# Performance work log

Hardware: AMD Instinct MI355X
Metric: run time of the kernel (lower is better)

The kernel has to match this reference:

```python
import jax, jax.numpy as jnp
import numpy as np

D = 768        # d_model
NH = 12        # n_head
HD = D // NH   # head_dim = 64
T = 8          # num_frames
SCALE = 1.0
LN_EPS = 1e-5


def _layer_norm(x, g, b):
    # fp16-safe LayerNorm: compute in fp32, cast back (matches LayerNorm subclass)
    x32 = x.astype(jnp.float32)
    mu = jnp.mean(x32, axis=-1, keepdims=True)
    var = jnp.mean(jnp.square(x32 - mu), axis=-1, keepdims=True)
    y = (x32 - mu) / jnp.sqrt(var + LN_EPS) * g + b
    return y.astype(x.dtype)


def _adapter(x, w1, b1, w2, b2):
    # Adapter with skip_connect=False: fc1 -> exact GELU -> fc2
    h = jax.nn.gelu(x @ w1.T + b1, approximate=False)
    return h @ w2.T + b2


def _mha(xq, ykv, w_in, b_in, w_out, b_out, need_weights=False):
    # xq: (Tx, N, D), ykv: (Ty, N, D); manual in-proj split like the torch code
    q = xq @ w_in[:D].T + b_in[:D]
    k = ykv @ w_in[D:2 * D].T + b_in[D:2 * D]
    v = ykv @ w_in[2 * D:].T + b_in[2 * D:]
    Tx, N = q.shape[0], q.shape[1]
    Ty = k.shape[0]
    q = q.reshape(Tx, N, NH, HD).transpose(1, 2, 0, 3)  # (N, H, Tx, hd)
    k = k.reshape(Ty, N, NH, HD).transpose(1, 2, 0, 3)
    v = v.reshape(Ty, N, NH, HD).transpose(1, 2, 0, 3)
    aff = jnp.einsum('nhqd,nhkd->nhqk', q, k) / jnp.asarray(HD ** 0.5, q.dtype)
    if need_weights:
        # torch does this under no_grad: sum over heads, exp, sum over (Tx*Ty)
        w = jax.lax.stop_gradient(
            jnp.sum(jnp.exp(jnp.sum(aff, axis=1)).reshape(N, -1), axis=-1))
    p = jax.nn.softmax(aff, axis=-1)
    out = jnp.einsum('nhqk,nhkd->nhqd', p, v)
    out = out.transpose(2, 0, 1, 3).reshape(Tx, N, D)
    out = out @ w_out.T + b_out
    if need_weights:
        return out, w
    return out


def setup_inputs() -> dict:
    key = jax.random.key(0)
    ks = jax.random.split(key, 12)
    DH = D // 4  # adapter hidden = 192

    def w(k, shape):
        return jax.random.normal(k, shape, jnp.float32) * 0.02

    z = lambda *s: jnp.zeros(s, jnp.float32)
    return {
        'x': jax.random.normal(ks[0], (197, 64, D), jnp.float32),
        'in_proj_w': w(ks[1], (3 * D, D)), 'in_proj_b': z(3 * D),
        'out_proj_w': w(ks[2], (D, D)), 'out_proj_b': z(D),
        'ln1_g': jnp.ones((D,), jnp.float32), 'ln1_b': z(D),
        'ln2_g': jnp.ones((D,), jnp.float32), 'ln2_b': z(D),
        'fc_w': w(ks[3], (4 * D, D)), 'fc_b': z(4 * D),
        'proj_w': w(ks[4], (D, 4 * D)), 'proj_b': z(D),
        'sa1_w': w(ks[5], (DH, D)), 'sa1_b': z(DH),
        'sa2_w': w(ks[6], (D, DH)), 'sa2_b': z(D),
        'ta1_w': w(ks[7], (DH, D)), 'ta1_b': z(DH),
        'ta2_w': w(ks[8], (D, DH)), 'ta2_b': z(D),
        'ma1_w': w(ks[9], (DH, D)), 'ma1_b': z(DH),
        'ma2_w': w(ks[10], (D, DH)), 'ma2_b': z(D),
    }


def reference(x, in_proj_w, in_proj_b, out_proj_w, out_proj_b,
              ln1_g, ln1_b, ln2_g, ln2_b, fc_w, fc_b, proj_w, proj_b,
              sa1_w, sa1_b, sa2_w, sa2_b, ta1_w, ta1_b, ta2_w, ta2_b,
              ma1_w, ma1_b, ma2_w, ma2_b):
    n, bt, d = x.shape
    b = bt // T
    # temporal attention on the class token: 'n (b t) d -> t (b n) d'
    ct = x[0]                                   # (bt, d)
    xt = ct.reshape(b, T, d).transpose(1, 0, 2)  # (T, b, d)
    xt = _mha(_layer_norm(xt, ln1_g, ln1_b), _layer_norm(xt, ln1_g, ln1_b),
              in_proj_w, in_proj_b, out_proj_w, out_proj_b)
    xt = _adapter(xt, ta1_w, ta1_b, ta2_w, ta2_b)
    xt = xt.transpose(1, 0, 2).reshape(1, bt, d)  # 't (b n) d -> n (b t) d'

    xln = _layer_norm(x, ln1_g, ln1_b)
    ori_attn, ori_w = _mha(xln, xln, in_proj_w, in_proj_b,
                           out_proj_w, out_proj_b, need_weights=True)
    crs_attn, crs_w = _mha(xln, xt, in_proj_w, in_proj_b,
                           out_proj_w, out_proj_b, need_weights=True)
    lam = (crs_w / (crs_w + ori_w))[None, :, None]  # (1, bt, 1)
    x = x + (1.0 - lam) * ori_attn \
          + SCALE * _adapter(lam * crs_attn, sa1_w, sa1_b, sa2_w, sa2_b)

    xn = _layer_norm(x, ln2_g, ln2_b)
    h = xn @ fc_w.T + fc_b
    h = h * jax.nn.sigmoid(1.702 * h)  # QuickGELU
    mlp_out = h @ proj_w.T + proj_b
    x = x + mlp_out + SCALE * _adapter(xn, ma1_w, ma1_b, ma2_w, ma2_b)
    return x
```

## Files before the change

### kernel.cpp

```cpp
#include <hip/hip_runtime.h>
#include <hip/hip_bf16.h>
#include <math.h>


typedef __attribute__((ext_vector_type(8))) short bf16x8;
typedef __attribute__((ext_vector_type(4))) float f32x4;

__device__ __forceinline__ float bf2f(short s) {
  unsigned u = ((unsigned)(unsigned short)s) << 16;
  float f;
  __builtin_memcpy(&f, &u, 4);
  return f;
}
__device__ __forceinline__ short f2bf(float f) {
  __hip_bfloat16 h = __float2bfloat16(f);
  short s;
  __builtin_memcpy(&s, &h, 2);
  return s;
}

__device__ __forceinline__ void gld16(void* lds, const void* g) {
  __builtin_amdgcn_global_load_lds(
      (const __attribute__((address_space(1))) unsigned int*)g,
      (__attribute__((address_space(3))) unsigned int*)lds, 16, 0, 0);
}

struct WPair { const float* s; short* d; int n; };
struct WArr { WPair p[10]; };

__global__ __launch_bounds__(256)
void convert_k(WArr a) {
  WPair w = a.p[blockIdx.y];
  for (int i = blockIdx.x * 256 + threadIdx.x; i < w.n; i += gridDim.x * 256)
    w.d[i] = f2bf(w.s[i]);
}

__global__ __launch_bounds__(256)
void ln_k(const float* __restrict__ in, const float* __restrict__ g,
          const float* __restrict__ b, short* __restrict__ out) {
  const int t = blockIdx.x;
  const float* xr = in + (size_t)t * 768;
  const int tid = threadIdx.x;
  float v0 = xr[tid], v1 = xr[tid + 256], v2 = xr[tid + 512];
  float s = v0 + v1 + v2;
#pragma unroll
  for (int m = 1; m < 64; m <<= 1) s += __shfl_xor(s, m);
  __shared__ float red[4];
  if ((tid & 63) == 0) red[tid >> 6] = s;
  __syncthreads();
  float mu = (red[0] + red[1] + red[2] + red[3]) * (1.f / 768.f);
  __syncthreads();
  float d0 = v0 - mu, d1 = v1 - mu, d2 = v2 - mu;
  float q = d0 * d0 + d1 * d1 + d2 * d2;
#pragma unroll
  for (int m = 1; m < 64; m <<= 1) q += __shfl_xor(q, m);
  if ((tid & 63) == 0) red[tid >> 6] = q;
  __syncthreads();
  float rstd = rsqrtf((red[0] + red[1] + red[2] + red[3]) * (1.f / 768.f) + 1e-5f);
  size_t o = (size_t)t * 768;
  out[o + tid]       = f2bf(d0 * rstd * g[tid]       + b[tid]);
  out[o + tid + 256] = f2bf(d1 * rstd * g[tid + 256] + b[tid + 256]);
  out[o + tid + 512] = f2bf(d2 * rstd * g[tid + 512] + b[tid + 512]);
}

template <int ACT, int EPI>
__global__ __launch_bounds__(256)
void gemm_k(const short* __restrict__ A, int lda,
            const short* __restrict__ W,
            const float* __restrict__ bias,
            short* __restrict__ outb, float* __restrict__ outf,
            const float* __restrict__ lam,
            int M, int N, int K) {
  __shared__ short As[64][40];
  __shared__ short Ws[64][40];
  const int tid = threadIdx.x;
  const int n0 = blockIdx.x * 64;
  const int m0 = blockIdx.y * 64;
  const int lane = tid & 63, w = tid >> 6;
  const int wr = w >> 1, wc = w & 1;
  const int g = lane >> 4, li = lane & 15;
  const int srow = tid >> 2, scol = (tid & 3) * 8;

  f32x4 acc[2][2];
#pragma unroll
  for (int i = 0; i < 2; i++)
#pragma unroll
    for (int j = 0; j < 2; j++) acc[i][j] = (f32x4){0.f, 0.f, 0.f, 0.f};

  const short* Aptr = A + (size_t)(m0 + srow) * lda + scol;
  const short* Wptr = W + (size_t)(n0 + srow) * K + scol;

  for (int kk = 0; kk < K; kk += 32) {
    __syncthreads();
    *(bf16x8*)&As[srow][scol] = *(const bf16x8*)(Aptr + kk);
    *(bf16x8*)&Ws[srow][scol] = *(const bf16x8*)(Wptr + kk);
    __syncthreads();
    bf16x8 a[2], b[2];
#pragma unroll
    for (int mi = 0; mi < 2; ++mi)
      a[mi] = *(const bf16x8*)&As[wr * 32 + mi * 16 + li][g * 8];
#pragma unroll
    for (int ni = 0; ni < 2; ++ni)
      b[ni] = *(const bf16x8*)&Ws[wc * 32 + ni * 16 + li][g * 8];
#pragma unroll
    for (int mi = 0; mi < 2; ++mi)
#pragma unroll
      for (int ni = 0; ni < 2; ++ni)
        acc[mi][ni] = __builtin_amdgcn_mfma_f32_16x16x32_bf16(
            a[mi], b[ni], acc[mi][ni], 0, 0, 0);
  }

#pragma unroll
  for (int mi = 0; mi < 2; ++mi)
#pragma unroll
    for (int ni = 0; ni < 2; ++ni)
#pragma unroll
      for (int r = 0; r < 4; ++r) {
        int row = m0 + wr * 32 + mi * 16 + g * 4 + r;
        int col = n0 + wc * 32 + ni * 16 + li;
        float v = acc[mi][ni][r];
        if (bias) v += bias[col];
        if (ACT == 1) v = v / (1.f + __expf(-1.702f * v));
        if (ACT == 2) v = 0.5f * v * (1.f + erff(v * 0.70710678118f));
        size_t idx = (size_t)row * N + col;
        if (EPI == 0) outb[idx] = f2bf(v);
        else if (EPI == 1) outf[idx] = v;
        else if (EPI == 5) outb[idx] = f2bf(v * lam[row]);
      }
}

template <int ACT, int EPI>
__global__ __launch_bounds__(256)
void gemm128_k(const short* __restrict__ A, int lda,
               const short* __restrict__ W,
               const float* __restrict__ bias,
               short* __restrict__ outb, float* __restrict__ outf,
               const float* __restrict__ lam,
               const float* __restrict__ addv,
               const float* __restrict__ resid,
               const short* __restrict__ A2, int lda2,
               const short* __restrict__ W2,
               const float* __restrict__ bias2, int K2,
               int M, int N, int K, int nx) {
  int nwg = gridDim.x;
  int orig = blockIdx.x;
  int q = nwg >> 3, r = nwg & 7;
  int xcd = orig & 7, cidx = orig >> 3;
  int wgid = (xcd < r ? xcd * (q + 1) : r * (q + 1) + (xcd - r) * q) + cidx;
  const int n0 = (wgid % nx) * 128;
  const int m0 = (wgid / nx) * 128;

  __shared__ short As[128][32];
  __shared__ short Ws[128][32];
  const int tid = threadIdx.x;
  const int w = tid >> 6, lane = tid & 63;
  const int g = lane >> 4, li = lane & 15;
  const int wr = w >> 1, wc = w & 1;

  const int srow = w * 16 + (lane >> 2);
  const int scol = (lane & 3) * 8;

  f32x4 acc[4][4];
#pragma unroll
  for (int i = 0; i < 4; i++)
#pragma unroll
    for (int j = 0; j < 4; j++) acc[i][j] = (f32x4){0.f, 0.f, 0.f, 0.f};

  int ar0 = m0 + srow;       if (ar0 > M - 1) ar0 = M - 1;
  int ar1 = m0 + 64 + srow;  if (ar1 > M - 1) ar1 = M - 1;
  const short* Ap0 = A + (size_t)ar0 * lda + scol;
  const short* Ap1 = A + (size_t)ar1 * lda + scol;
  const short* Wp0 = W + (size_t)(n0 + srow) * K + scol;
  const short* Wp1 = W + (size_t)(n0 + 64 + srow) * K + scol;
  short* lA0 = &As[w * 16][0];
  short* lA1 = &As[64 + w * 16][0];
  short* lW0 = &Ws[w * 16][0];
  short* lW1 = &Ws[64 + w * 16][0];

  for (int kk = 0; kk < K; kk += 32) {
    __syncthreads();
    gld16(lA0, Ap0 + kk);
    gld16(lA1, Ap1 + kk);
    gld16(lW0, Wp0 + kk);
    gld16(lW1, Wp1 + kk);
    __syncthreads();
    bf16x8 a[4], b[4];
#pragma unroll
    for (int mi = 0; mi < 4; ++mi)
      a[mi] = *(const bf16x8*)&As[wr * 64 + mi * 16 + li][g * 8];
#pragma unroll
    for (int ni = 0; ni < 4; ++ni)
      b[ni] = *(const bf16x8*)&Ws[wc * 64 + ni * 16 + li][g * 8];
#pragma unroll
    for (int mi = 0; mi < 4; ++mi)
#pragma unroll
      for (int ni = 0; ni < 4; ++ni)
        acc[mi][ni] = __builtin_amdgcn_mfma_f32_16x16x32_bf16(
            a[mi], b[ni], acc[mi][ni], 0, 0, 0);
  }

  if (A2) {
    const short* Bp0 = A2 + (size_t)ar0 * lda2 + scol;
    const short* Bp1 = A2 + (size_t)ar1 * lda2 + scol;
    const short* Vp0 = W2 + (size_t)(n0 + srow) * K2 + scol;
    const short* Vp1 = W2 + (size_t)(n0 + 64 + srow) * K2 + scol;
    for (int kk = 0; kk < K2; kk += 32) {
      __syncthreads();
      gld16(lA0, Bp0 + kk);
      gld16(lA1, Bp1 + kk);
      gld16(lW0, Vp0 + kk);
      gld16(lW1, Vp1 + kk);
      __syncthreads();
      bf16x8 a[4], b[4];
#pragma unroll
      for (int mi = 0; mi < 4; ++mi)
        a[mi] = *(const bf16x8*)&As[wr * 64 + mi * 16 + li][g * 8];
#pragma unroll
      for (int ni = 0; ni < 4; ++ni)
        b[ni] = *(const bf16x8*)&Ws[wc * 64 + ni * 16 + li][g * 8];
#pragma unroll
      for (int mi = 0; mi < 4; ++mi)
#pragma unroll
        for (int ni = 0; ni < 4; ++ni)
          acc[mi][ni] = __builtin_amdgcn_mfma_f32_16x16x32_bf16(
              a[mi], b[ni], acc[mi][ni], 0, 0, 0);
    }
  }

#pragma unroll
  for (int mi = 0; mi < 4; ++mi)
#pragma unroll
    for (int ni = 0; ni < 4; ++ni)
#pragma unroll
      for (int r = 0; r < 4; ++r) {
        int row = m0 + wr * 64 + mi * 16 + g * 4 + r;
        int col = n0 + wc * 64 + ni * 16 + li;
        if (row >= M) continue;
        float v = acc[mi][ni][r];
        if (bias) v += bias[col];
        if (bias2) v += bias2[col];
        if (ACT == 1) v = v / (1.f + __expf(-1.702f * v));
        if (ACT == 2) v = 0.5f * v * (1.f + erff(v * 0.70710678118f));
        size_t idx = (size_t)row * N + col;
        if (EPI == 0) outb[idx] = f2bf(v);
        else if (EPI == 2) {
          float l = lam[row & 63];
          outf[idx] = resid[idx] + (1.f - l) * v + addv[(size_t)(row & 63) * 768 + col];
        } else if (EPI == 6) outf[idx] = resid[idx] + v;
      }
}

__global__ __launch_bounds__(256)
void attn_k(const short* __restrict__ qkv, short* __restrict__ attn_out) {
  const int n = blockIdx.x;
  const int h = blockIdx.y;
  const int tid = threadIdx.x;
  const int lane = tid & 63, w = tid >> 6;
  const int g = lane >> 4, li = lane & 15;

  __shared__ short Vt[64][232];
  __shared__ short Pl[4][16][232];

  {
    const int d = tid & 63;
    for (int key = tid >> 6; key < 224; key += 4) {
      short v = 0;
      if (key < 197)
        v = qkv[(size_t)(key * 64 + n) * 2304 + 1536 + h * 64 + d];
      Vt[d][key] = v;
    }
  }
  __syncthreads();

  const short* Qb = qkv + (size_t)n * 2304 + h * 64;
  const short* Kb = Qb + 768;

  for (int mt = w; mt < 13; mt += 4) {
    const int m0 = mt * 16;
    int arow = m0 + li;
    if (arow > 196) arow = 196;
    bf16x8 a0 = *(const bf16x8*)(Qb + (size_t)arow * 147456 + g * 8);
    bf16x8 a1 = *(const bf16x8*)(Qb + (size_t)arow * 147456 + 32 + g * 8);

    float s[13][4];
#pragma unroll
    for (int nt = 0; nt < 13; ++nt) {
      int kc = nt * 16 + li;
      if (kc > 196) kc = 196;
      bf16x8 b0 = *(const bf16x8*)(Kb + (size_t)kc * 147456 + g * 8);
      bf16x8 b1 = *(const bf16x8*)(Kb + (size_t)kc * 147456 + 32 + g * 8);
      f32x4 acc = (f32x4){0.f, 0.f, 0.f, 0.f};
      acc = __builtin_amdgcn_mfma_f32_16x16x32_bf16(a0, b0, acc, 0, 0, 0);
      acc = __builtin_amdgcn_mfma_f32_16x16x32_bf16(a1, b1, acc, 0, 0, 0);
#pragma unroll
      for (int r = 0; r < 4; ++r) s[nt][r] = acc[r] * 0.125f;
    }

#pragma unroll
    for (int r = 0; r < 4; ++r) {
      float mx = -1e30f;
#pragma unroll
      for (int nt = 0; nt < 13; ++nt) {
        if (nt * 16 + li >= 197) s[nt][r] = -1e30f;
        mx = fmaxf(mx, s[nt][r]);
      }
      mx = fmaxf(mx, __shfl_xor(mx, 1));
      mx = fmaxf(mx, __shfl_xor(mx, 2));
      mx = fmaxf(mx, __shfl_xor(mx, 4));
      mx = fmaxf(mx, __shfl_xor(mx, 8));
      float sum = 0.f;
#pragma unroll
      for (int nt = 0; nt < 13; ++nt) {
        float e = (s[nt][r] <= -1e29f) ? 0.f : __expf(s[nt][r] - mx);
        s[nt][r] = e;
        sum += e;
      }
      sum += __shfl_xor(sum, 1);
      sum += __shfl_xor(sum, 2);
      sum += __shfl_xor(sum, 4);
      sum += __shfl_xor(sum, 8);
      float inv = 1.f / sum;
#pragma unroll
      for (int nt = 0; nt < 13; ++nt) s[nt][r] *= inv;
    }

#pragma unroll
    for (int r = 0; r < 4; ++r) {
      int row = g * 4 + r;
#pragma unroll
      for (int nt = 0; nt < 13; ++nt)
        Pl[w][row][nt * 16 + li] = f2bf(s[nt][r]);
      Pl[w][row][208 + li] = 0;
    }
    asm volatile("s_waitcnt lgkmcnt(0)" ::: "memory");
    __builtin_amdgcn_sched_barrier(0);

    f32x4 o[4];
#pragma unroll
    for (int ni = 0; ni < 4; ++ni) o[ni] = (f32x4){0.f, 0.f, 0.f, 0.f};
#pragma unroll
    for (int kk = 0; kk < 7; ++kk) {
      bf16x8 pa = *(const bf16x8*)&Pl[w][li][kk * 32 + g * 8];
#pragma unroll
      for (int ni = 0; ni < 4; ++ni) {
        bf16x8 vb = *(const bf16x8*)&Vt[ni * 16 + li][kk * 32 + g * 8];
        o[ni] = __builtin_amdgcn_mfma_f32_16x16x32_bf16(pa, vb, o[ni], 0, 0, 0);
      }
    }
#pragma unroll
    for (int ni = 0; ni < 4; ++ni)
#pragma unroll
      for (int r = 0; r < 4; ++r) {
        int prow = m0 + g * 4 + r;
        if (prow < 197)
          attn_out[(size_t)(prow * 64 + n) * 768 + h * 64 + ni * 16 + li] =
              f2bf(o[ni][r]);
      }
  }
}

__global__ __launch_bounds__(256)
void lam_part_k(const short* __restrict__ qkv, float* __restrict__ eo_part) {
  const int n = blockIdx.x;
  const int mt = blockIdx.y;
  const int tid = threadIdx.x;
  const int lane = tid & 63, w = tid >> 6;
  const int g = lane >> 4, li = lane & 15;
  const short* Qb = qkv + (size_t)n * 2304;
  const short* Kb = Qb + 768;

  int arow = mt * 16 + li;
  if (arow > 196) arow = 196;
  const short* Ap = Qb + (size_t)arow * 147456;

  bf16x8 a[24];
#pragma unroll
  for (int s = 0; s < 24; ++s)
    a[s] = *(const bf16x8*)(Ap + s * 32 + g * 8);

  float eo = 0.f;
  for (int nt = w; nt < 13; nt += 4) {
    int kc = nt * 16 + li;
    if (kc > 196) kc = 196;
    const short* Bp = Kb + (size_t)kc * 147456;
    f32x4 acc = (f32x4){0.f, 0.f, 0.f, 0.f};
#pragma unroll
    for (int s = 0; s < 24; ++s) {
      bf16x8 b = *(const bf16x8*)(Bp + s * 32 + g * 8);
      acc = __builtin_amdgcn_mfma_f32_16x16x32_bf16(a[s], b, acc, 0, 0, 0);
    }
#pragma unroll
    for (int r = 0; r < 4; ++r) {
      int prow = mt * 16 + g * 4 + r;
      int col = nt * 16 + li;
      if (prow < 197 && col < 197) eo += __expf(acc[r] * 0.125f);
    }
  }

#pragma unroll
  for (int m = 1; m < 64; m <<= 1) eo += __shfl_xor(eo, m);
  __shared__ float red[4];
  if (lane == 0) red[w] = eo;
  __syncthreads();
  if (tid == 0)
    eo_part[n * 13 + mt] = red[0] + red[1] + red[2] + red[3];
}

__global__ __launch_bounds__(64)
void lam_fin_k(const short* __restrict__ qkv, const short* __restrict__ kvt,
               const float* __restrict__ eo_part, float* __restrict__ lam) {
  const int n = blockIdx.x;
  const int lane = threadIdx.x;
  const short* kt = kvt + (size_t)n * 1536;

  float ec = 0.f;
  for (int p = lane; p < 197; p += 64) {
    const short* qp = qkv + (size_t)n * 2304 + (size_t)p * 147456;
    float dot = 0.f;
    for (int d0 = 0; d0 < 768; d0 += 8) {
      bf16x8 qa = *(const bf16x8*)(qp + d0);
      bf16x8 ka = *(const bf16x8*)(kt + d0);
#pragma unroll
      for (int j = 0; j < 8; ++j) dot += bf2f(qa[j]) * bf2f(ka[j]);
    }
    ec += __expf(dot * 0.125f);
  }
#pragma unroll
  for (int m = 1; m < 64; m <<= 1) ec += __shfl_xor(ec, m);

  if (lane == 0) {
    float eo = 0.f;
#pragma unroll
    for (int t = 0; t < 13; ++t) eo += eo_part[n * 13 + t];
    lam[n] = ec / (ec + eo);
  }
}

__global__ __launch_bounds__(64)
void tattn_k(const short* __restrict__ qkv, short* __restrict__ attn_t) {
  const int bb = blockIdx.x, h = blockIdx.y;
  const int tid = threadIdx.x;
  __shared__ float sm[8][9];
  {
    const int tt = tid >> 3, ss = tid & 7;
    const short* q = qkv + (size_t)(bb * 8 + tt) * 2304 + h * 64;
    const short* k = qkv + (size_t)(bb * 8 + ss) * 2304 + 768 + h * 64;
    float dot = 0.f;
#pragma unroll
    for (int d = 0; d < 64; d += 8) {
      bf16x8 qa = *(const bf16x8*)(q + d);
      bf16x8 ka = *(const bf16x8*)(k + d);
#pragma unroll
      for (int j = 0; j < 8; ++j) dot += bf2f(qa[j]) * bf2f(ka[j]);
    }
    sm[tt][ss] = dot * 0.125f;
  }
  __syncthreads();
  if (tid < 8) {
    float mx = -1e30f;
#pragma unroll
    for (int s2 = 0; s2 < 8; ++s2) mx = fmaxf(mx, sm[tid][s2]);
    float sum = 0.f;
#pragma unroll
    for (int s2 = 0; s2 < 8; ++s2) {
      float e = __expf(sm[tid][s2] - mx);
      sm[tid][s2] = e;
      sum += e;
    }
    float inv = 1.f / sum;
#pragma unroll
    for (int s2 = 0; s2 < 8; ++s2) sm[tid][s2] *= inv;
  }
  __syncthreads();
  {
    const int d = tid;
    float v[8];
#pragma unroll
    for (int s2 = 0; s2 < 8; ++s2)
      v[s2] = bf2f(qkv[(size_t)(bb * 8 + s2) * 2304 + 1536 + h * 64 + d]);
#pragma unroll
    for (int tt = 0; tt < 8; ++tt) {
      float o = 0.f;
#pragma unroll
      for (int s2 = 0; s2 < 8; ++s2) o += sm[tt][s2] * v[s2];
      attn_t[(size_t)(bb * 8 + tt) * 768 + h * 64 + d] = f2bf(o);
    }
  }
}

extern "C" void kernel_launch(void* const* d_in, const int* in_sizes, int n_in,
                              void* d_out, int out_size, void* d_ws,
                              size_t ws_size, hipStream_t stream) {
  (void)in_sizes; (void)n_in; (void)out_size; (void)ws_size;

  const float* x          = (const float*)d_in[0];
  const float* in_proj_w  = (const float*)d_in[1];
  const float* in_proj_b  = (const float*)d_in[2];
  const float* out_proj_w = (const float*)d_in[3];
  const float* out_proj_b = (const float*)d_in[4];
  const float* ln1_g      = (const float*)d_in[5];
  const float* ln1_b      = (const float*)d_in[6];
  const float* ln2_g      = (const float*)d_in[7];
  const float* ln2_b      = (const float*)d_in[8];
  const float* fc_w       = (const float*)d_in[9];
  const float* fc_b       = (const float*)d_in[10];
  const float* proj_w     = (const float*)d_in[11];
  const float* proj_b     = (const float*)d_in[12];
  const float* sa1_w      = (const float*)d_in[13];
  const float* sa1_b      = (const float*)d_in[14];
  const float* sa2_w      = (const float*)d_in[15];
  const float* sa2_b      = (const float*)d_in[16];
  const float* ta1_w      = (const float*)d_in[17];
  const float* ta1_b      = (const float*)d_in[18];
  const float* ta2_w      = (const float*)d_in[19];
  const float* ta2_b      = (const float*)d_in[20];
  const float* ma1_w      = (const float*)d_in[21];
  const float* ma1_b      = (const float*)d_in[22];
  const float* ma2_w      = (const float*)d_in[23];
  const float* ma2_b      = (const float*)d_in[24];

  char* ws = (char*)d_ws;
  short* xln  = (short*)(ws + 0);
  short* qkv  = (short*)(ws + 19365888);
  short* hbuf = (short*)(ws + 0);
  short* attn = (short*)(ws + 77463552);
  short* h2   = (short*)(ws + 77463552);
  float* x1   = (float*)(ws + 96829440);
  short* xn   = (short*)(ws + 135561216);

  char* wreg = ws + 154927104;
  short* w_inproj  = (short*)(wreg + 0);
  short* w_outproj = (short*)(wreg + 3538944);
  short* w_fc      = (short*)(wreg + 4718592);
  short* w_proj    = (short*)(wreg + 9437184);
  short* w_sa1     = (short*)(wreg + 14155776);
  short* w_sa2     = (short*)(wreg + 14450688);
  short* w_ta1     = (short*)(wreg + 14745600);
  short* w_ta2     = (short*)(wreg + 15040512);
  short* w_ma1     = (short*)(wreg + 15335424);
  short* w_ma2     = (short*)(wreg + 15630336);

  char* sm = ws + 170852352;
  short* attn_t  = (short*)(sm + 0);
  short* tproj   = (short*)(sm + 98304);
  short* th      = (short*)(sm + 196608);
  short* xt_out  = (short*)(sm + 221184);
  short* kv_t    = (short*)(sm + 319488);
  short* a_in    = (short*)(sm + 516096);
  short* sa_h    = (short*)(sm + 614400);
  float* sa_out  = (float*)(sm + 638976);
  float* lam     = (float*)(sm + 835584);
  float* eo_part = (float*)(sm + 835840);

  float* out = (float*)d_out;

  WArr arr;
  arr.p[0] = {in_proj_w,  w_inproj,  2304 * 768};
  arr.p[1] = {out_proj_w, w_outproj, 768 * 768};
  arr.p[2] = {fc_w,       w_fc,      3072 * 768};
  arr.p[3] = {proj_w,     w_proj,    768 * 3072};
  arr.p[4] = {sa1_w,      w_sa1,     192 * 768};
  arr.p[5] = {sa2_w,      w_sa2,     768 * 192};
  arr.p[6] = {ta1_w,      w_ta1,     192 * 768};
  arr.p[7] = {ta2_w,      w_ta2,     768 * 192};
  arr.p[8] = {ma1_w,      w_ma1,     192 * 768};
  arr.p[9] = {ma2_w,      w_ma2,     768 * 192};
  convert_k<<<dim3(128, 10), 256, 0, stream>>>(arr);

  ln_k<<<12608, 256, 0, stream>>>(x, ln1_g, ln1_b, xln);

  gemm128_k<0, 0><<<18 * 99, 256, 0, stream>>>(
      xln, 768, w_inproj, in_proj_b, qkv, nullptr, nullptr, nullptr, nullptr,
      nullptr, 0, nullptr, nullptr, 0, 12608, 2304, 768, 18);

  lam_part_k<<<dim3(64, 13), 256, 0, stream>>>(qkv, eo_part);

  tattn_k<<<dim3(8, 12), 64, 0, stream>>>(qkv, attn_t);

  gemm_k<0, 0><<<dim3(12, 1), 256, 0, stream>>>(
      attn_t, 768, w_outproj, out_proj_b, tproj, nullptr, nullptr, 64, 768, 768);
  gemm_k<2, 0><<<dim3(3, 1), 256, 0, stream>>>(
      tproj, 768, w_ta1, ta1_b, th, nullptr, nullptr, 64, 192, 768);
  gemm_k<0, 0><<<dim3(12, 1), 256, 0, stream>>>(
      th, 192, w_ta2, ta2_b, xt_out, nullptr, nullptr, 64, 768, 192);
  gemm_k<0, 0><<<dim3(24, 1), 256, 0, stream>>>(
      xt_out, 768, w_inproj + 768 * 768, in_proj_b + 768, kv_t, nullptr,
      nullptr, 64, 1536, 768);

  attn_k<<<dim3(64, 12), 256, 0, stream>>>(qkv, attn);

  lam_fin_k<<<64, 64, 0, stream>>>(qkv, kv_t, eo_part, lam);

  gemm_k<0, 5><<<dim3(12, 1), 256, 0, stream>>>(
      kv_t + 768, 1536, w_outproj, out_proj_b, a_in, nullptr, lam, 64, 768, 768);
  gemm_k<2, 0><<<dim3(3, 1), 256, 0, stream>>>(
      a_in, 768, w_sa1, sa1_b, sa_h, nullptr, nullptr, 64, 192, 768);
  gemm_k<0, 1><<<dim3(12, 1), 256, 0, stream>>>(
      sa_h, 192, w_sa2, sa2_b, nullptr, sa_out, nullptr, 64, 768, 192);

  gemm128_k<0, 2><<<6 * 99, 256, 0, stream>>>(
      attn, 768, w_outproj, out_proj_b, nullptr, x1, lam, sa_out, x,
      nullptr, 0, nullptr, nullptr, 0, 12608, 768, 768, 6);

  ln_k<<<12608, 256, 0, stream>>>(x1, ln2_g, ln2_b, xn);

  gemm128_k<1, 0><<<24 * 99, 256, 0, stream>>>(
      xn, 768, w_fc, fc_b, hbuf, nullptr, nullptr, nullptr, nullptr,
      nullptr, 0, nullptr, nullptr, 0, 12608, 3072, 768, 24);
  gemm_k<2, 0><<<dim3(3, 197), 256, 0, stream>>>(
      xn, 768, w_ma1, ma1_b, h2, nullptr, nullptr, 12608, 192, 768);

  gemm128_k<0, 6><<<6 * 99, 256, 0, stream>>>(
      hbuf, 3072, w_proj, proj_b, nullptr, out, nullptr, nullptr, x1,
      h2, 192, w_ma2, ma2_b, 192, 12608, 768, 3072, 6);
}
```

Measured before the change: 761.6 us.

## Triple-buffer LDS in the 128x128 GEMM with async prefetch two stages ahead

The 128-tile GEMM now uses three LDS buffers and issues global-to-LDS loads two k-steps ahead. Per-step waits use vmcnt counting and a single barrier instead of two __syncthreads. The second (adapter) K-loop is merged into the same pipelined loop through a unified stage index. The goal is to hide global load latency behind MFMA work, at the cost of triple the LDS footprint, which may reduce occupancy.

```diff
diff --git a/kernel.cpp b/kernel.cpp
--- a/kernel.cpp
+++ b/kernel.cpp
@@ -131,17 +131,17 @@
 
 template <int ACT, int EPI>
 __global__ __launch_bounds__(256)
-void gemm128_k(const short* __restrict__ A, int lda,
-               const short* __restrict__ W,
-               const float* __restrict__ bias,
-               short* __restrict__ outb, float* __restrict__ outf,
-               const float* __restrict__ lam,
-               const float* __restrict__ addv,
-               const float* __restrict__ resid,
-               const short* __restrict__ A2, int lda2,
-               const short* __restrict__ W2,
-               const float* __restrict__ bias2, int K2,
-               int M, int N, int K, int nx) {
+void gemm128p_k(const short* __restrict__ A, int lda,
+                const short* __restrict__ W,
+                const float* __restrict__ bias,
+                short* __restrict__ outb, float* __restrict__ outf,
+                const float* __restrict__ lam,
+                const float* __restrict__ addv,
+                const float* __restrict__ resid,
+                const short* __restrict__ A2, int lda2,
+                const short* __restrict__ W2,
+                const float* __restrict__ bias2, int K2,
+                int M, int N, int K, int nx) {
   int nwg = gridDim.x;
   int orig = blockIdx.x;
   int q = nwg >> 3, r = nwg & 7;
@@ -150,8 +150,8 @@
   const int n0 = (wgid % nx) * 128;
   const int m0 = (wgid / nx) * 128;
 
-  __shared__ short As[128][32];
-  __shared__ short Ws[128][32];
+  __shared__ short As[3][128][32];
+  __shared__ short Ws[3][128][32];
   const int tid = threadIdx.x;
   const int w = tid >> 6, lane = tid & 63;
   const int g = lane >> 4, li = lane & 15;
@@ -172,59 +172,64 @@
   const short* Ap1 = A + (size_t)ar1 * lda + scol;
   const short* Wp0 = W + (size_t)(n0 + srow) * K + scol;
   const short* Wp1 = W + (size_t)(n0 + 64 + srow) * K + scol;
-  short* lA0 = &As[w * 16][0];
-  short* lA1 = &As[64 + w * 16][0];
-  short* lW0 = &Ws[w * 16][0];
-  short* lW1 = &Ws[64 + w * 16][0];
-
-  for (int kk = 0; kk < K; kk += 32) {
-    __syncthreads();
-    gld16(lA0, Ap0 + kk);
-    gld16(lA1, Ap1 + kk);
-    gld16(lW0, Wp0 + kk);
-    gld16(lW1, Wp1 + kk);
-    __syncthreads();
+  const short* A2b = A2 ? A2 : A;
+  const short* W2b = W2 ? W2 : W;
+  const short* Bp0 = A2b + (size_t)ar0 * lda2 + scol;
+  const short* Bp1 = A2b + (size_t)ar1 * lda2 + scol;
+  const short* Vp0 = W2b + (size_t)(n0 + srow) * K2 + scol;
+  const short* Vp1 = W2b + (size_t)(n0 + 64 + srow) * K2 + scol;
+
+  const int ks1 = K >> 5;
+  const int ks2 = A2 ? (K2 >> 5) : 0;
+  const int total = ks1 + ks2;
+
+  auto STAGE = [&](int s, int bi) {
+    if (s < ks1) {
+      const int kk = s * 32;
+      gld16(&As[bi][w * 16][0],      Ap0 + kk);
+      gld16(&As[bi][64 + w * 16][0], Ap1 + kk);
+      gld16(&Ws[bi][w * 16][0],      Wp0 + kk);
+      gld16(&Ws[bi][64 + w * 16][0], Wp1 + kk);
+    } else {
+      const int kk = (s - ks1) * 32;
+      gld16(&As[bi][w * 16][0],      Bp0 + kk);
+      gld16(&As[bi][64 + w * 16][0], Bp1 + kk);
+      gld16(&Ws[bi][w * 16][0],      Vp0 + kk);
+      gld16(&Ws[bi][64 + w * 16][0], Vp1 + kk);
+    }
+  };
+
+  STAGE(0, 0);
+  STAGE(1, 1);
+
+  int bi = 0;
+  for (int t = 0; t < total; ++t) {
+    if (t + 1 < total)
+      asm volatile("s_waitcnt vmcnt(4)" ::: "memory");
+    else
+      asm volatile("s_waitcnt vmcnt(0)" ::: "memory");
+    __builtin_amdgcn_s_barrier();
+
+    int nb = bi + 2; if (nb >= 3) nb -= 3;
+    if (t + 2 < total) STAGE(t + 2, nb);
+
     bf16x8 a[4], b[4];
 #pragma unroll
     for (int mi = 0; mi < 4; ++mi)
-      a[mi] = *(const bf16x8*)&As[wr * 64 + mi * 16 + li][g * 8];
+      a[mi] = *(const bf16x8*)&As[bi][wr * 64 + mi * 16 + li][g * 8];
 #pragma unroll
     for (int ni = 0; ni < 4; ++ni)
-      b[ni] = *(const bf16x8*)&Ws[wc * 64 + ni * 16 + li][g * 8];
+      b[ni] = *(const bf16x8*)&Ws[bi][wc * 64 + ni * 16 + li][g * 8];
+    asm volatile("s_waitcnt lgkmcnt(0)" ::: "memory");
+    __builtin_amdgcn_sched_barrier(0);
 #pragma unroll
     for (int mi = 0; mi < 4; ++mi)
 #pragma unroll
       for (int ni = 0; ni < 4; ++ni)
         acc[mi][ni] = __builtin_amdgcn_mfma_f32_16x16x32_bf16(
             a[mi], b[ni], acc[mi][ni], 0, 0, 0);
-  }
-
-  if (A2) {
-    const short* Bp0 = A2 + (size_t)ar0 * lda2 + scol;
-    const short* Bp1 = A2 + (size_t)ar1 * lda2 + scol;
-    const short* Vp0 = W2 + (size_t)(n0 + srow) * K2 + scol;
-    const short* Vp1 = W2 + (size_t)(n0 + 64 + srow) * K2 + scol;
-    for (int kk = 0; kk < K2; kk += 32) {
-      __syncthreads();
-      gld16(lA0, Bp0 + kk);
-      gld16(lA1, Bp1 + kk);
-      gld16(lW0, Vp0 + kk);
-      gld16(lW1, Vp1 + kk);
-      __syncthreads();
-      bf16x8 a[4], b[4];
-#pragma unroll
-      for (int mi = 0; mi < 4; ++mi)
-        a[mi] = *(const bf16x8*)&As[wr * 64 + mi * 16 + li][g * 8];
-#pragma unroll
-      for (int ni = 0; ni < 4; ++ni)
-        b[ni] = *(const bf16x8*)&Ws[wc * 64 + ni * 16 + li][g * 8];
-#pragma unroll
-      for (int mi = 0; mi < 4; ++mi)
-#pragma unroll
-        for (int ni = 0; ni < 4; ++ni)
-          acc[mi][ni] = __builtin_amdgcn_mfma_f32_16x16x32_bf16(
-              a[mi], b[ni], acc[mi][ni], 0, 0, 0);
-    }
+
+    bi = bi + 1; if (bi >= 3) bi = 0;
   }
 
 #pragma unroll
@@ -569,9 +574,9 @@
 
   ln_k<<<12608, 256, 0, stream>>>(x, ln1_g, ln1_b, xln);
 
-  gemm128_k<0, 0><<<18 * 99, 256, 0, stream>>>(
+  gemm128p_k<0, 0><<<18 * 99, 256, 0, stream>>>(
       xln, 768, w_inproj, in_proj_b, qkv, nullptr, nullptr, nullptr, nullptr,
-      nullptr, 0, nullptr, nullptr, 0, 12608, 2304, 768, 18);
+      nullptr, 0, nullptr, nullptr, 32, 12608, 2304, 768, 18);
 
   lam_part_k<<<dim3(64, 13), 256, 0, stream>>>(qkv, eo_part);
 
@@ -598,19 +603,19 @@
   gemm_k<0, 1><<<dim3(12, 1), 256, 0, stream>>>(
       sa_h, 192, w_sa2, sa2_b, nullptr, sa_out, nullptr, 64, 768, 192);
 
-  gemm128_k<0, 2><<<6 * 99, 256, 0, stream>>>(
+  gemm128p_k<0, 2><<<6 * 99, 256, 0, stream>>>(
       attn, 768, w_outproj, out_proj_b, nullptr, x1, lam, sa_out, x,
-      nullptr, 0, nullptr, nullptr, 0, 12608, 768, 768, 6);
+      nullptr, 0, nullptr, nullptr, 32, 12608, 768, 768, 6);
 
   ln_k<<<12608, 256, 0, stream>>>(x1, ln2_g, ln2_b, xn);
 
-  gemm128_k<1, 0><<<24 * 99, 256, 0, stream>>>(
+  gemm128p_k<1, 0><<<24 * 99, 256, 0, stream>>>(
       xn, 768, w_fc, fc_b, hbuf, nullptr, nullptr, nullptr, nullptr,
-      nullptr, 0, nullptr, nullptr, 0, 12608, 3072, 768, 24);
+      nullptr, 0, nullptr, nullptr, 32, 12608, 3072, 768, 24);
   gemm_k<2, 0><<<dim3(3, 197), 256, 0, stream>>>(
       xn, 768, w_ma1, ma1_b, h2, nullptr, nullptr, 12608, 192, 768);
 
-  gemm128_k<0, 6><<<6 * 99, 256, 0, stream>>>(
+  gemm128p_k<0, 6><<<6 * 99, 256, 0, stream>>>(
       hbuf, 3072, w_proj, proj_b, nullptr, out, nullptr, nullptr, x1,
       h2, 192, w_ma2, ma2_b, 192, 12608, 768, 3072, 6);
 }
```

After: 731.5 us. 3.9% less time.
